# Optimization experiments

Hardware: AMD Instinct MI355X
Metric: run time of the kernel (lower is better)

The kernel has to match this reference:

```python
import math
import jax, jax.numpy as jnp
import numpy as np

B, L, DIM, H = 2, 2048, 1024, 16
HD = DIM // H  # 64
EPS = 1e-6


def _rms_norm(x):
    # x: [..., d] float32; no learned weight (trainable=False)
    norm = jax.lax.rsqrt(jnp.mean(jnp.square(x), axis=-1, keepdims=True) + EPS)
    return x * norm


def _apply_rotary(x, cos, sin):
    # x: [b, h, l, d]; cos/sin: [1, 1, l, d//2]
    d = x.shape[-1] // 2
    x1, x2 = x[..., :d], x[..., d:]
    y1 = x1 * cos + x2 * sin
    y2 = -x1 * sin + x2 * cos
    return jnp.concatenate([y1, y2], axis=-1)


def setup_inputs() -> dict:
    key = jax.random.key(0)
    ks = jax.random.split(key, 6)
    s = 0.02
    return {
        "x": jax.random.normal(ks[0], (B, L, DIM), dtype=jnp.float32),
        "v_0": jax.random.normal(ks[1], (B, H, L, HD), dtype=jnp.float32),
        "rope_cos": jnp.cos(jax.random.normal(ks[2], (1, 1, L, HD // 2), dtype=jnp.float32)),
        "rope_sin": jnp.sin(jax.random.normal(ks[2], (1, 1, L, HD // 2), dtype=jnp.float32)),
        "qkv_w": jax.random.normal(ks[3], (3 * DIM, DIM), dtype=jnp.float32) * s,
        "proj_w": jax.random.normal(ks[4], (DIM, DIM), dtype=jnp.float32) * s,
        "lambda_param": jnp.full((1,), 0.5, dtype=jnp.float32),
    }


def reference(x, v_0, rope_cos, rope_sin, qkv_w, proj_w, lambda_param):
    b, l, dim = x.shape
    # QKV projection (no bias): [b, l, 3*dim]
    qkv = jnp.einsum('bld,ed->ble', x, qkv_w)
    # rearrange 'b l (k h d) -> k b h l d'
    qkv = qkv.reshape(b, l, 3, H, HD).transpose(2, 0, 3, 1, 4)
    q, k, v = qkv[0], qkv[1], qkv[2]
    # residual-v blend
    lam = lambda_param.reshape(())
    v = lam * v + (1.0 - lam) * v_0
    # RoPE (done in float32, inputs already float32)
    q = _apply_rotary(q, rope_cos, rope_sin)
    k = _apply_rotary(k, rope_cos, rope_sin)
    # dynamic softmax temperature
    ratio = math.sqrt(math.log(l) / math.log(1040.0))
    k = k * ratio
    # QKNorm (RMSNorm over head_dim, no weight)
    q = _rms_norm(q)
    k = _rms_norm(k)
    # scaled dot product attention
    scale = 1.0 / math.sqrt(HD)
    scores = jnp.einsum('bhqd,bhkd->bhqk', q, k) * scale
    attn = jax.nn.softmax(scores, axis=-1)
    out = jnp.einsum('bhqk,bhkd->bhqd', attn, v)
    # 'b h l d -> b l (h d)' then output projection (no bias)
    out = out.transpose(0, 2, 1, 3).reshape(b, l, dim)
    out = jnp.einsum('bld,ed->ble', out, proj_w)
    return (out, v)
```

## Files before the change

### kernel.cpp

```cpp
#include <hip/hip_runtime.h>

typedef _Float16 f16;
typedef _Float16 f16x8 __attribute__((ext_vector_type(8)));
typedef _Float16 f16x4 __attribute__((ext_vector_type(4)));
typedef float f32x4 __attribute__((ext_vector_type(4)));

#define MFMA32(a, b, c) __builtin_amdgcn_mfma_f32_16x16x32_f16((a), (b), (c), 0, 0, 0)
#define MFMA16(a, b, c) __builtin_amdgcn_mfma_f32_16x16x16f16((a), (b), (c), 0, 0, 0)

constexpr int Bs = 2, Ls = 2048, DIM = 1024, NH = 16, HD = 64;
constexpr int BL = Bs * Ls;
constexpr float EPSV = 1e-6f;
constexpr float SCL2 = 0.125f * 1.44269504f;

__global__ void cvt_all_kernel(const float* __restrict__ x, const float* __restrict__ wq,
                               const float* __restrict__ wp, f16* __restrict__ xf,
                               f16* __restrict__ wqf, f16* __restrict__ wpf) {
  constexpr int NX4 = BL * DIM / 4;
  constexpr int NW4 = 3 * DIM * DIM / 4;
  int i = blockIdx.x * blockDim.x + threadIdx.x;
  const float4* src;
  f16x4* dst;
  int j;
  if (i < NX4) {
    src = (const float4*)x; dst = (f16x4*)xf; j = i;
  } else if (i < NX4 + NW4) {
    src = (const float4*)wq; dst = (f16x4*)wqf; j = i - NX4;
  } else {
    src = (const float4*)wp; dst = (f16x4*)wpf; j = i - NX4 - NW4;
  }
  float4 a = src[j];
  f16x4 o = {(f16)a.x, (f16)a.y, (f16)a.z, (f16)a.w};
  dst[j] = o;
}

__global__ __launch_bounds__(256) void qkv_gemm_kernel(
    const f16* __restrict__ A, const f16* __restrict__ W,
    const float* __restrict__ v0,
    const float* __restrict__ rcos, const float* __restrict__ rsin,
    const float* __restrict__ lamp,
    f16* __restrict__ qb, f16* __restrict__ kb, f16* __restrict__ vbT,
    float* __restrict__ vout) {
  constexpr int K = DIM;
  __shared__ alignas(16) f16 sA[2][128 * 64];
  __shared__ alignas(16) f16 sB[2][128 * 64];
  const int tid = threadIdx.x;
  const int w = tid >> 6, lane = tid & 63, ln = lane & 15, quad = lane >> 4;
  const int wm = w >> 1, wn = w & 1;
  const int m0 = blockIdx.y * 128, n0 = blockIdx.x * 128;

  const f16* gA[4];
  const f16* gB[4];
#pragma unroll
  for (int s = 0; s < 4; ++s) {
    int lc = tid + s * 256;
    int r = lc >> 3;
    int c = ((lc & 7) ^ (r & 7)) * 8;
    gA[s] = A + (size_t)(m0 + r) * K + c;
    gB[s] = W + (size_t)(n0 + r) * K + c;
  }

  f16x8 ra[4], rb[4];
  auto load = [&](int k0) {
#pragma unroll
    for (int s = 0; s < 4; ++s) {
      ra[s] = *(const f16x8*)(gA[s] + k0);
      rb[s] = *(const f16x8*)(gB[s] + k0);
    }
  };
  auto store = [&](int buf) {
#pragma unroll
    for (int s = 0; s < 4; ++s) {
      int lc = tid + s * 256;
      *(f16x8*)&sA[buf][lc * 8] = ra[s];
      *(f16x8*)&sB[buf][lc * 8] = rb[s];
    }
  };

  f32x4 acc[4][4] = {};
  load(0);
  store(0);
  __syncthreads();

  for (int it = 0; it < K / 64; ++it) {
    const int cur = it & 1;
    if (it + 1 < K / 64) load((it + 1) * 64);
#pragma unroll
    for (int kk = 0; kk < 2; ++kk) {
      f16x8 a[4];
#pragma unroll
      for (int mi = 0; mi < 4; ++mi) {
        int r = wm * 64 + mi * 16 + ln;
        a[mi] = *(const f16x8*)&sA[cur][r * 64 + (((kk * 4 + quad) ^ (r & 7)) * 8)];
      }
#pragma unroll
      for (int ni = 0; ni < 4; ++ni) {
        int r = wn * 64 + ni * 16 + ln;
        f16x8 b = *(const f16x8*)&sB[cur][r * 64 + (((kk * 4 + quad) ^ (r & 7)) * 8)];
#pragma unroll
        for (int mi = 0; mi < 4; ++mi) acc[mi][ni] = MFMA32(a[mi], b, acc[mi][ni]);
      }
    }
    if (it + 1 < K / 64) store(cur ^ 1);
    __syncthreads();
  }

  const int nb = n0 + wn * 64;
  const int nsec = nb >> 10;
  const int h = (nb & 1023) >> 6;

  if (nsec == 2) {
    const float lam = lamp[0];
#pragma unroll
    for (int mi = 0; mi < 4; ++mi) {
#pragma unroll
      for (int rg = 0; rg < 4; ++rg) {
        int row = m0 + wm * 64 + mi * 16 + quad * 4 + rg;
        int b = row >> 11, l = row & 2047;
        size_t base = ((size_t)(b * NH + h) * Ls + l) * HD;
        size_t tb = ((size_t)(b * NH + h) * HD) * Ls + l;
#pragma unroll
        for (int ni = 0; ni < 4; ++ni) {
          int d = ni * 16 + ln;
          float vnew = lam * acc[mi][ni][rg] + (1.0f - lam) * v0[base + d];
          vout[base + d] = vnew;
          vbT[tb + (size_t)d * Ls] = (f16)vnew;
        }
      }
    }
  } else {
    f16* dst = nsec ? kb : qb;
    const float ratio = sqrtf(logf(2048.0f) / logf(1040.0f));
#pragma unroll
    for (int mi = 0; mi < 4; ++mi) {
#pragma unroll
      for (int rg = 0; rg < 4; ++rg) {
        int row = m0 + wm * 64 + mi * 16 + quad * 4 + rg;
        int b = row >> 11, l = row & 2047;
        float vals[4];
#pragma unroll
        for (int ni = 0; ni < 4; ++ni) vals[ni] = acc[mi][ni][rg];
#pragma unroll
        for (int t = 0; t < 2; ++t) {
          int j = t * 16 + ln;
          float c = rcos[l * 32 + j], s = rsin[l * 32 + j];
          float x1 = vals[t], x2 = vals[t + 2];
          vals[t] = x1 * c + x2 * s;
          vals[t + 2] = -x1 * s + x2 * c;
        }
        if (nsec) {
#pragma unroll
          for (int ni = 0; ni < 4; ++ni) vals[ni] *= ratio;
        }
        float ms = vals[0] * vals[0] + vals[1] * vals[1] + vals[2] * vals[2] + vals[3] * vals[3];
        ms += __shfl_xor(ms, 1);
        ms += __shfl_xor(ms, 2);
        ms += __shfl_xor(ms, 4);
        ms += __shfl_xor(ms, 8);
        float rn = rsqrtf(ms * (1.0f / 64.0f) + EPSV);
        size_t base = ((size_t)(b * NH + h) * Ls + l) * HD;
#pragma unroll
        for (int ni = 0; ni < 4; ++ni) dst[base + ni * 16 + ln] = (f16)(vals[ni] * rn);
      }
    }
  }
}

__global__ __launch_bounds__(256) void flash_kernel(
    const f16* __restrict__ qg, const f16* __restrict__ kg, const f16* __restrict__ vtg,
    f16* __restrict__ ao) {
  __shared__ alignas(16) f16 sK[2][64 * 64];
  __shared__ alignas(16) f16 sVT[2][64 * 64];
  const int tid = threadIdx.x;
  const int w = tid >> 6, lane = tid & 63, ln = lane & 15, quad = lane >> 4;
  const int bx = blockIdx.x;
  const int qt = bx & 15, h = (bx >> 4) & 15, b = bx >> 8;
  const f16* Qh = qg + (size_t)(b * NH + h) * Ls * HD;
  const f16* Kh = kg + (size_t)(b * NH + h) * Ls * HD;
  const f16* VTh = vtg + (size_t)(b * NH + h) * HD * Ls;
  const int q0 = qt * 128;

  f16x8 aq[2][2];
#pragma unroll
  for (int st = 0; st < 2; ++st)
#pragma unroll
    for (int kk = 0; kk < 2; ++kk)
      aq[st][kk] = *(const f16x8*)&Qh[(size_t)(q0 + w * 32 + st * 16 + ln) * HD + kk * 32 + quad * 8];

  f16x8 kr[2], vr[2];
  auto loadKV = [&](int k0) {
#pragma unroll
    for (int s = 0; s < 2; ++s) {
      int ch = tid + s * 256, r = ch >> 3, cg = (ch & 7) * 8;
      kr[s] = *(const f16x8*)&Kh[(size_t)(k0 + r) * HD + cg];
      vr[s] = *(const f16x8*)&VTh[(size_t)r * Ls + k0 + cg];
    }
  };
  auto stageKV = [&](int buf) {
#pragma unroll
    for (int s = 0; s < 2; ++s) {
      int ch = tid + s * 256, r = ch >> 3;
      int po = r * 64 + (((ch & 7) ^ (r & 7)) * 8);
      *(f16x8*)&sK[buf][po] = kr[s];
      *(f16x8*)&sVT[buf][po] = vr[s];
    }
  };

  f32x4 O[2][4] = {};
  float rsum[2] = {0.f, 0.f};

  loadKV(0);
  stageKV(0);
  __syncthreads();

  for (int kt = 0; kt < 32; ++kt) {
    const int cur = kt & 1;
    if (kt < 31) loadKV((kt + 1) * 64);

    f16x4 pf[2][4];
#pragma unroll
    for (int nt = 0; nt < 4; ++nt) {
      int r = nt * 16 + ln;
      f16x8 kf0 = *(const f16x8*)&sK[cur][r * 64 + ((quad ^ (r & 7)) * 8)];
      f16x8 kf1 = *(const f16x8*)&sK[cur][r * 64 + (((4 + quad) ^ (r & 7)) * 8)];
#pragma unroll
      for (int st = 0; st < 2; ++st) {
        f32x4 z = {};
        z = MFMA32(kf0, aq[st][0], z);
        z = MFMA32(kf1, aq[st][1], z);
        float p0 = exp2f(z[0] * SCL2);
        float p1 = exp2f(z[1] * SCL2);
        float p2 = exp2f(z[2] * SCL2);
        float p3 = exp2f(z[3] * SCL2);
        rsum[st] += (p0 + p1) + (p2 + p3);
        f16x4 pk = {(f16)p0, (f16)p1, (f16)p2, (f16)p3};
        pf[st][nt] = pk;
      }
    }

#pragma unroll
    for (int dt = 0; dt < 4; ++dt) {
      int row = dt * 16 + ln;
#pragma unroll
      for (int nt = 0; nt < 4; ++nt) {
        int cv = nt * 2 + (quad >> 1);
        f16x4 vf = *(const f16x4*)&sVT[cur][row * 64 + ((cv ^ (row & 7)) * 8) + (quad & 1) * 4];
#pragma unroll
        for (int st = 0; st < 2; ++st) O[st][dt] = MFMA16(pf[st][nt], vf, O[st][dt]);
      }
    }

    if (kt < 31) stageKV(cur ^ 1);
    __syncthreads();
  }

#pragma unroll
  for (int st = 0; st < 2; ++st) {
    float rs = rsum[st];
    rs += __shfl_xor(rs, 16);
    rs += __shfl_xor(rs, 32);
#pragma unroll
    for (int rg = 0; rg < 4; ++rg) {
      float inv = 1.0f / __shfl(rs, quad * 4 + rg);
      int q = q0 + w * 32 + st * 16 + quad * 4 + rg;
      size_t orow = ((size_t)b * Ls + q) * DIM + h * HD;
#pragma unroll
      for (int dt = 0; dt < 4; ++dt)
        ao[orow + dt * 16 + ln] = (f16)(O[st][dt][rg] * inv);
    }
  }
}

__global__ __launch_bounds__(256) void proj_gemm_kernel(
    const f16* __restrict__ A, const f16* __restrict__ W, float* __restrict__ out) {
  constexpr int K = DIM;
  __shared__ alignas(16) f16 sA[2][64 * 64];
  __shared__ alignas(16) f16 sB[2][128 * 64];
  const int tid = threadIdx.x;
  const int w = tid >> 6, lane = tid & 63, ln = lane & 15, quad = lane >> 4;
  const int wm = w >> 1, wn = w & 1;
  const int m0 = blockIdx.y * 64, n0 = blockIdx.x * 128;

  const f16* gA[2];
  const f16* gB[4];
#pragma unroll
  for (int s = 0; s < 2; ++s) {
    int lc = tid + s * 256;
    int r = lc >> 3;
    gA[s] = A + (size_t)(m0 + r) * K + (((lc & 7) ^ (r & 7)) * 8);
  }
#pragma unroll
  for (int s = 0; s < 4; ++s) {
    int lc = tid + s * 256;
    int r = lc >> 3;
    gB[s] = W + (size_t)(n0 + r) * K + (((lc & 7) ^ (r & 7)) * 8);
  }

  f16x8 ra[2], rb[4];
  auto load = [&](int k0) {
#pragma unroll
    for (int s = 0; s < 2; ++s) ra[s] = *(const f16x8*)(gA[s] + k0);
#pragma unroll
    for (int s = 0; s < 4; ++s) rb[s] = *(const f16x8*)(gB[s] + k0);
  };
  auto store = [&](int buf) {
#pragma unroll
    for (int s = 0; s < 2; ++s) *(f16x8*)&sA[buf][(tid + s * 256) * 8] = ra[s];
#pragma unroll
    for (int s = 0; s < 4; ++s) *(f16x8*)&sB[buf][(tid + s * 256) * 8] = rb[s];
  };

  f32x4 acc[2][4] = {};
  load(0);
  store(0);
  __syncthreads();

  for (int it = 0; it < K / 64; ++it) {
    const int cur = it & 1;
    if (it + 1 < K / 64) load((it + 1) * 64);
#pragma unroll
    for (int kk = 0; kk < 2; ++kk) {
      f16x8 a[2];
#pragma unroll
      for (int mi = 0; mi < 2; ++mi) {
        int r = wm * 32 + mi * 16 + ln;
        a[mi] = *(const f16x8*)&sA[cur][r * 64 + (((kk * 4 + quad) ^ (r & 7)) * 8)];
      }
#pragma unroll
      for (int ni = 0; ni < 4; ++ni) {
        int r = wn * 64 + ni * 16 + ln;
        f16x8 b = *(const f16x8*)&sB[cur][r * 64 + (((kk * 4 + quad) ^ (r & 7)) * 8)];
#pragma unroll
        for (int mi = 0; mi < 2; ++mi) acc[mi][ni] = MFMA32(a[mi], b, acc[mi][ni]);
      }
    }
    if (it + 1 < K / 64) store(cur ^ 1);
    __syncthreads();
  }

#pragma unroll
  for (int mi = 0; mi < 2; ++mi) {
#pragma unroll
    for (int rg = 0; rg < 4; ++rg) {
      int row = m0 + wm * 32 + mi * 16 + quad * 4 + rg;
      size_t o = (size_t)row * DIM + n0 + wn * 64;
#pragma unroll
      for (int ni = 0; ni < 4; ++ni) out[o + ni * 16 + ln] = acc[mi][ni][rg];
    }
  }
}

extern "C" void kernel_launch(void* const* d_in, const int* in_sizes, int n_in,
                              void* d_out, int out_size, void* d_ws, size_t ws_size,
                              hipStream_t stream) {
  (void)in_sizes; (void)n_in; (void)out_size; (void)ws_size;
  const float* x = (const float*)d_in[0];
  const float* v0 = (const float*)d_in[1];
  const float* rcos = (const float*)d_in[2];
  const float* rsin = (const float*)d_in[3];
  const float* wqkv = (const float*)d_in[4];
  const float* wproj = (const float*)d_in[5];
  const float* lamp = (const float*)d_in[6];
  float* out = (float*)d_out;
  float* vout = out + (size_t)BL * DIM;

  char* p = (char*)d_ws;
  auto take = [&](size_t n) { char* q = p; p += ((n + 255) / 256) * 256; return q; };
  f16* xf = (f16*)take((size_t)BL * DIM * 2);
  f16* wqf = (f16*)take((size_t)3 * DIM * DIM * 2);
  f16* wpf = (f16*)take((size_t)DIM * DIM * 2);
  f16* qb = (f16*)take((size_t)BL * DIM * 2);
  f16* kb = (f16*)take((size_t)BL * DIM * 2);
  f16* vbT = (f16*)take((size_t)BL * DIM * 2);
  f16* ao = xf;

  constexpr int NCVT4 = (BL * DIM + 3 * DIM * DIM + DIM * DIM) / 4;
  cvt_all_kernel<<<dim3(NCVT4 / 256), dim3(256), 0, stream>>>(x, wqkv, wproj, xf, wqf, wpf);

  qkv_gemm_kernel<<<dim3(3 * DIM / 128, BL / 128), dim3(256), 0, stream>>>(
      xf, wqf, v0, rcos, rsin, lamp, qb, kb, vbT, vout);

  flash_kernel<<<dim3(Bs * NH * (Ls / 128)), dim3(256), 0, stream>>>(qb, kb, vbT, ao);

  proj_gemm_kernel<<<dim3(DIM / 128, BL / 64), dim3(256), 0, stream>>>(ao, wpf, out);
}
```

Before: 241.9 us.

## Use direct global-to-LDS async loads in GEMMs, fold softmax scale into Q, permute V layout

Both GEMM kernels now stage tiles with global_load_lds straight into a single swizzled 32-wide LDS buffer, replacing the register-staged double buffer. The goal is lower register pressure and LDS footprint, in exchange for losing overlap between global loads and MFMA work. The softmax scale is folded into Q normalization, which removes a multiply per score in the flash kernel. V^T is stored key-permuted so the PV step can read 8-wide vectors and issue two MFMA16s per load.

```diff
diff --git a/kernel.cpp b/kernel.cpp
--- a/kernel.cpp
+++ b/kernel.cpp
@@ -12,6 +12,16 @@
 constexpr int BL = Bs * Ls;
 constexpr float EPSV = 1e-6f;
 constexpr float SCL2 = 0.125f * 1.44269504f;
+
+__device__ __forceinline__ void async16(void* lds, const void* g) {
+  __builtin_amdgcn_global_load_lds((const __attribute__((address_space(1))) void*)g,
+                                   (__attribute__((address_space(3))) void*)lds, 16, 0, 0);
+}
+
+__device__ __forceinline__ int sw32(int r, int q) {
+  int p = r >> 1;
+  return p * 64 + ((((r & 1) * 4 + q) ^ (p & 7)) * 8);
+}
 
 __global__ void cvt_all_kernel(const float* __restrict__ x, const float* __restrict__ wq,
                                const float* __restrict__ wp, f16* __restrict__ xf,
@@ -42,66 +52,44 @@
     f16* __restrict__ qb, f16* __restrict__ kb, f16* __restrict__ vbT,
     float* __restrict__ vout) {
   constexpr int K = DIM;
-  __shared__ alignas(16) f16 sA[2][128 * 64];
-  __shared__ alignas(16) f16 sB[2][128 * 64];
+  __shared__ alignas(16) f16 sA[128 * 32];
+  __shared__ alignas(16) f16 sB[128 * 32];
   const int tid = threadIdx.x;
   const int w = tid >> 6, lane = tid & 63, ln = lane & 15, quad = lane >> 4;
   const int wm = w >> 1, wn = w & 1;
   const int m0 = blockIdx.y * 128, n0 = blockIdx.x * 128;
 
-  const f16* gA[4];
-  const f16* gB[4];
-#pragma unroll
-  for (int s = 0; s < 4; ++s) {
+  const f16* gA[2];
+  const f16* gB[2];
+#pragma unroll
+  for (int s = 0; s < 2; ++s) {
     int lc = tid + s * 256;
-    int r = lc >> 3;
-    int c = ((lc & 7) ^ (r & 7)) * 8;
-    gA[s] = A + (size_t)(m0 + r) * K + c;
-    gB[s] = W + (size_t)(n0 + r) * K + c;
-  }
-
-  f16x8 ra[4], rb[4];
-  auto load = [&](int k0) {
-#pragma unroll
-    for (int s = 0; s < 4; ++s) {
-      ra[s] = *(const f16x8*)(gA[s] + k0);
-      rb[s] = *(const f16x8*)(gB[s] + k0);
-    }
-  };
-  auto store = [&](int buf) {
-#pragma unroll
-    for (int s = 0; s < 4; ++s) {
-      int lc = tid + s * 256;
-      *(f16x8*)&sA[buf][lc * 8] = ra[s];
-      *(f16x8*)&sB[buf][lc * 8] = rb[s];
-    }
-  };
+    int p = lc >> 3, g = (lc & 7) ^ (p & 7);
+    int r = 2 * p + (g >> 2), ce = (g & 3) * 8;
+    gA[s] = A + (size_t)(m0 + r) * K + ce;
+    gB[s] = W + (size_t)(n0 + r) * K + ce;
+  }
 
   f32x4 acc[4][4] = {};
-  load(0);
-  store(0);
-  __syncthreads();
-
-  for (int it = 0; it < K / 64; ++it) {
-    const int cur = it & 1;
-    if (it + 1 < K / 64) load((it + 1) * 64);
-#pragma unroll
-    for (int kk = 0; kk < 2; ++kk) {
-      f16x8 a[4];
-#pragma unroll
-      for (int mi = 0; mi < 4; ++mi) {
-        int r = wm * 64 + mi * 16 + ln;
-        a[mi] = *(const f16x8*)&sA[cur][r * 64 + (((kk * 4 + quad) ^ (r & 7)) * 8)];
-      }
-#pragma unroll
-      for (int ni = 0; ni < 4; ++ni) {
-        int r = wn * 64 + ni * 16 + ln;
-        f16x8 b = *(const f16x8*)&sB[cur][r * 64 + (((kk * 4 + quad) ^ (r & 7)) * 8)];
-#pragma unroll
-        for (int mi = 0; mi < 4; ++mi) acc[mi][ni] = MFMA32(a[mi], b, acc[mi][ni]);
-      }
-    }
-    if (it + 1 < K / 64) store(cur ^ 1);
+
+  for (int it = 0; it < 32; ++it) {
+    const int k0 = it * 32;
+#pragma unroll
+    for (int s = 0; s < 2; ++s) {
+      async16(&sA[(tid + s * 256) * 8], gA[s] + k0);
+      async16(&sB[(tid + s * 256) * 8], gB[s] + k0);
+    }
+    __syncthreads();
+    f16x8 a[4];
+#pragma unroll
+    for (int mi = 0; mi < 4; ++mi)
+      a[mi] = *(const f16x8*)&sA[sw32(wm * 64 + mi * 16 + ln, quad)];
+#pragma unroll
+    for (int ni = 0; ni < 4; ++ni) {
+      f16x8 b = *(const f16x8*)&sB[sw32(wn * 64 + ni * 16 + ln, quad)];
+#pragma unroll
+      for (int mi = 0; mi < 4; ++mi) acc[mi][ni] = MFMA32(a[mi], b, acc[mi][ni]);
+    }
     __syncthreads();
   }
 
@@ -118,7 +106,9 @@
         int row = m0 + wm * 64 + mi * 16 + quad * 4 + rg;
         int b = row >> 11, l = row & 2047;
         size_t base = ((size_t)(b * NH + h) * Ls + l) * HD;
-        size_t tb = ((size_t)(b * NH + h) * HD) * Ls + l;
+        int key = l & 63;
+        int sidx = ((key >> 2) & 3) * 16 + (key >> 4) * 4 + (key & 3);
+        size_t tb = ((size_t)(b * NH + h) * HD) * Ls + (l & ~63) + sidx;
 #pragma unroll
         for (int ni = 0; ni < 4; ++ni) {
           int d = ni * 16 + ln;
@@ -131,6 +121,7 @@
   } else {
     f16* dst = nsec ? kb : qb;
     const float ratio = sqrtf(logf(2048.0f) / logf(1040.0f));
+    const float post = nsec ? 1.0f : SCL2;
 #pragma unroll
     for (int mi = 0; mi < 4; ++mi) {
 #pragma unroll
@@ -157,7 +148,7 @@
         ms += __shfl_xor(ms, 2);
         ms += __shfl_xor(ms, 4);
         ms += __shfl_xor(ms, 8);
-        float rn = rsqrtf(ms * (1.0f / 64.0f) + EPSV);
+        float rn = rsqrtf(ms * (1.0f / 64.0f) + EPSV) * post;
         size_t base = ((size_t)(b * NH + h) * Ls + l) * HD;
 #pragma unroll
         for (int ni = 0; ni < 4; ++ni) dst[base + ni * 16 + ln] = (f16)(vals[ni] * rn);
@@ -228,10 +219,10 @@
         f32x4 z = {};
         z = MFMA32(kf0, aq[st][0], z);
         z = MFMA32(kf1, aq[st][1], z);
-        float p0 = exp2f(z[0] * SCL2);
-        float p1 = exp2f(z[1] * SCL2);
-        float p2 = exp2f(z[2] * SCL2);
-        float p3 = exp2f(z[3] * SCL2);
+        float p0 = exp2f(z[0]);
+        float p1 = exp2f(z[1]);
+        float p2 = exp2f(z[2]);
+        float p3 = exp2f(z[3]);
         rsum[st] += (p0 + p1) + (p2 + p3);
         f16x4 pk = {(f16)p0, (f16)p1, (f16)p2, (f16)p3};
         pf[st][nt] = pk;
@@ -242,11 +233,15 @@
     for (int dt = 0; dt < 4; ++dt) {
       int row = dt * 16 + ln;
 #pragma unroll
-      for (int nt = 0; nt < 4; ++nt) {
-        int cv = nt * 2 + (quad >> 1);
-        f16x4 vf = *(const f16x4*)&sVT[cur][row * 64 + ((cv ^ (row & 7)) * 8) + (quad & 1) * 4];
-#pragma unroll
-        for (int st = 0; st < 2; ++st) O[st][dt] = MFMA16(pf[st][nt], vf, O[st][dt]);
+      for (int nt2 = 0; nt2 < 2; ++nt2) {
+        f16x8 vf = *(const f16x8*)&sVT[cur][row * 64 + (((quad * 2 + nt2) ^ (row & 7)) * 8)];
+        f16x4 vlo = {vf[0], vf[1], vf[2], vf[3]};
+        f16x4 vhi = {vf[4], vf[5], vf[6], vf[7]};
+#pragma unroll
+        for (int st = 0; st < 2; ++st) {
+          O[st][dt] = MFMA16(pf[st][2 * nt2], vlo, O[st][dt]);
+          O[st][dt] = MFMA16(pf[st][2 * nt2 + 1], vhi, O[st][dt]);
+        }
       }
     }
 
@@ -274,67 +269,44 @@
 __global__ __launch_bounds__(256) void proj_gemm_kernel(
     const f16* __restrict__ A, const f16* __restrict__ W, float* __restrict__ out) {
   constexpr int K = DIM;
-  __shared__ alignas(16) f16 sA[2][64 * 64];
-  __shared__ alignas(16) f16 sB[2][128 * 64];
+  __shared__ alignas(16) f16 sA[64 * 32];
+  __shared__ alignas(16) f16 sB[128 * 32];
   const int tid = threadIdx.x;
   const int w = tid >> 6, lane = tid & 63, ln = lane & 15, quad = lane >> 4;
   const int wm = w >> 1, wn = w & 1;
   const int m0 = blockIdx.y * 64, n0 = blockIdx.x * 128;
 
-  const f16* gA[2];
-  const f16* gB[4];
+  const f16* gA;
+  {
+    int p = tid >> 3, g = (tid & 7) ^ (p & 7);
+    gA = A + (size_t)(m0 + 2 * p + (g >> 2)) * K + (g & 3) * 8;
+  }
+  const f16* gB[2];
 #pragma unroll
   for (int s = 0; s < 2; ++s) {
     int lc = tid + s * 256;
-    int r = lc >> 3;
-    gA[s] = A + (size_t)(m0 + r) * K + (((lc & 7) ^ (r & 7)) * 8);
-  }
-#pragma unroll
-  for (int s = 0; s < 4; ++s) {
-    int lc = tid + s * 256;
-    int r = lc >> 3;
-    gB[s] = W + (size_t)(n0 + r) * K + (((lc & 7) ^ (r & 7)) * 8);
-  }
-
-  f16x8 ra[2], rb[4];
-  auto load = [&](int k0) {
-#pragma unroll
-    for (int s = 0; s < 2; ++s) ra[s] = *(const f16x8*)(gA[s] + k0);
-#pragma unroll
-    for (int s = 0; s < 4; ++s) rb[s] = *(const f16x8*)(gB[s] + k0);
-  };
-  auto store = [&](int buf) {
-#pragma unroll
-    for (int s = 0; s < 2; ++s) *(f16x8*)&sA[buf][(tid + s * 256) * 8] = ra[s];
-#pragma unroll
-    for (int s = 0; s < 4; ++s) *(f16x8*)&sB[buf][(tid + s * 256) * 8] = rb[s];
-  };
+    int p = lc >> 3, g = (lc & 7) ^ (p & 7);
+    gB[s] = W + (size_t)(n0 + 2 * p + (g >> 2)) * K + (g & 3) * 8;
+  }
 
   f32x4 acc[2][4] = {};
-  load(0);
-  store(0);
-  __syncthreads();
-
-  for (int it = 0; it < K / 64; ++it) {
-    const int cur = it & 1;
-    if (it + 1 < K / 64) load((it + 1) * 64);
-#pragma unroll
-    for (int kk = 0; kk < 2; ++kk) {
-      f16x8 a[2];
-#pragma unroll
-      for (int mi = 0; mi < 2; ++mi) {
-        int r = wm * 32 + mi * 16 + ln;
-        a[mi] = *(const f16x8*)&sA[cur][r * 64 + (((kk * 4 + quad) ^ (r & 7)) * 8)];
-      }
-#pragma unroll
-      for (int ni = 0; ni < 4; ++ni) {
-        int r = wn * 64 + ni * 16 + ln;
-        f16x8 b = *(const f16x8*)&sB[cur][r * 64 + (((kk * 4 + quad) ^ (r & 7)) * 8)];
-#pragma unroll
-        for (int mi = 0; mi < 2; ++mi) acc[mi][ni] = MFMA32(a[mi], b, acc[mi][ni]);
-      }
-    }
-    if (it + 1 < K / 64) store(cur ^ 1);
+
+  for (int it = 0; it < 32; ++it) {
+    const int k0 = it * 32;
+    async16(&sA[tid * 8], gA + k0);
+#pragma unroll
+    for (int s = 0; s < 2; ++s) async16(&sB[(tid + s * 256) * 8], gB[s] + k0);
+    __syncthreads();
+    f16x8 a[2];
+#pragma unroll
+    for (int mi = 0; mi < 2; ++mi)
+      a[mi] = *(const f16x8*)&sA[sw32(wm * 32 + mi * 16 + ln, quad)];
+#pragma unroll
+    for (int ni = 0; ni < 4; ++ni) {
+      f16x8 b = *(const f16x8*)&sB[sw32(wn * 64 + ni * 16 + ln, quad)];
+#pragma unroll
+      for (int mi = 0; mi < 2; ++mi) acc[mi][ni] = MFMA32(a[mi], b, acc[mi][ni]);
+    }
     __syncthreads();
   }
 
```

New measurement: 239.1 us. No clear change (-1.2%).
